# Performance work log

Hardware: AMD Instinct MI355X
Metric: run time of the kernel (lower is better)

Reference implementation:

```python
import jax, jax.numpy as jnp
import numpy as np


def setup_inputs() -> dict:
    key = jax.random.key(0)
    k1, k2, k3 = jax.random.split(key, 3)
    d = 256
    x = jax.random.normal(k1, (8, 2048, d), dtype=jnp.float32)
    # torch nn.Linear(d, d, bias=False) weights, shape [out, in]
    Wq = jax.random.normal(k2, (d, d), dtype=jnp.float32) * (d ** -0.5)
    Wk = jax.random.normal(k3, (d, d), dtype=jnp.float32) * (d ** -0.5)
    return {"x": x, "Wq": Wq, "Wk": Wk}


def reference(x, Wq, Wk):
    # q = x @ Wq^T, k = x @ Wk^T (torch Linear convention), v = x (raw context)
    d = x.shape[-1]
    scale = d ** -0.5
    q = jnp.einsum('bnd,ed->bne', x, Wq)
    k = jnp.einsum('bnd,ed->bne', x, Wk)
    sim = jnp.einsum('bid,bjd->bij', q, k) * scale  # [b, n, n]
    attn = jax.nn.softmax(sim, axis=-1)
    out = jnp.einsum('bij,bjd->bid', attn, x)
    return out
```

## Files before the change

### kernel.cpp

```cpp
#include <hip/hip_runtime.h>
#include <hip/hip_bf16.h>

#define BB 8
#define NN 2048
#define DD 256

typedef _Float16 half8 __attribute__((ext_vector_type(8)));
typedef _Float16 half4 __attribute__((ext_vector_type(4)));
typedef float f32x4 __attribute__((ext_vector_type(4)));
typedef unsigned int uint4v __attribute__((ext_vector_type(4)));

#define GLDS(gsrc, ldst) __builtin_amdgcn_global_load_lds( \
    (const __attribute__((address_space(1))) void*)(gsrc), \
    (__attribute__((address_space(3))) void*)(ldst), 16, 0, 0)

__device__ __forceinline__ half8 cvt8(const float* __restrict__ p) {
    f32x4 a = *(const f32x4*)p;
    f32x4 b = *(const f32x4*)(p + 4);
    half8 h;
    h[0] = (_Float16)a[0]; h[1] = (_Float16)a[1];
    h[2] = (_Float16)a[2]; h[3] = (_Float16)a[3];
    h[4] = (_Float16)b[0]; h[5] = (_Float16)b[1];
    h[6] = (_Float16)b[2]; h[7] = (_Float16)b[3];
    return h;
}

__global__ void __launch_bounds__(256)
qk_proj(const float* __restrict__ x, const float* __restrict__ Wq,
        const float* __restrict__ Wk, _Float16* __restrict__ qh,
        _Float16* __restrict__ kh, _Float16* __restrict__ xT) {
    __shared__ __align__(16) _Float16 Wql[16][264];
    __shared__ __align__(16) _Float16 Wkl[16][264];
    const int tid = threadIdx.x;
    const int wave = tid >> 6, lane = tid & 63;
    const int g = lane >> 4, l16 = lane & 15;
    const int rowblk = blockIdx.x >> 1, thalf = blockIdx.x & 1;
    const size_t r0 = ((size_t)rowblk * 4 + wave) * 16;

    half8 xa[8];
#pragma unroll
    for (int c = 0; c < 8; ++c)
        xa[c] = cvt8(x + (r0 + l16) * DD + c * 32 + g * 8);

    {
        const int gt = (int)(r0 + l16);
        const int bb = gt >> 11, nn = gt & 2047;
        _Float16* xtb = xT + (size_t)bb * DD * NN + nn;
        if (thalf == 0) {
#pragma unroll
            for (int c = 0; c < 4; ++c)
#pragma unroll
                for (int j = 0; j < 8; ++j)
                    xtb[(size_t)(c * 32 + g * 8 + j) * NN] = xa[c][j];
        } else {
#pragma unroll
            for (int c = 4; c < 8; ++c)
#pragma unroll
                for (int j = 0; j < 8; ++j)
                    xtb[(size_t)(c * 32 + g * 8 + j) * NN] = xa[c][j];
        }
    }

    for (int i = 0; i < 8; ++i) {
        const int t = thalf * 8 + i;
        __syncthreads();
        {
            const int sel = tid >> 7;
            const int tt  = tid & 127;
            const int row = tt >> 3;
            const int col = (tt & 7) * 32;
            const float* src = (sel ? Wk : Wq) + (size_t)(t * 16 + row) * DD + col;
            _Float16* dst = sel ? &Wkl[row][col] : &Wql[row][col];
#pragma unroll
            for (int j = 0; j < 4; ++j)
                *(half8*)(dst + j * 8) = cvt8(src + j * 8);
        }
        __syncthreads();
        f32x4 aq = {0.f, 0.f, 0.f, 0.f}, ak = {0.f, 0.f, 0.f, 0.f};
#pragma unroll
        for (int c = 0; c < 8; ++c) {
            half8 bq = *(const half8*)&Wql[l16][c * 32 + g * 8];
            half8 bk = *(const half8*)&Wkl[l16][c * 32 + g * 8];
            aq = __builtin_amdgcn_mfma_f32_16x16x32_f16(xa[c], bq, aq, 0, 0, 0);
            ak = __builtin_amdgcn_mfma_f32_16x16x32_f16(xa[c], bk, ak, 0, 0, 0);
        }
#pragma unroll
        for (int r = 0; r < 4; ++r) {
            size_t row = r0 + g * 4 + r;
            qh[row * DD + t * 16 + l16] = (_Float16)(aq[r] * 0.0625f);
            kh[row * DD + t * 16 + l16] = (_Float16)ak[r];
        }
    }
}

__global__ void __launch_bounds__(512, 2)
attn(const _Float16* __restrict__ qh, const _Float16* __restrict__ kh,
     const _Float16* __restrict__ xT, float* __restrict__ out,
     _Float16* __restrict__ Op, float* __restrict__ ml, int lgS) {
    __shared__ __align__(16) _Float16 Kl[2][32 * 256];
    __shared__ __align__(16) _Float16 Vl[2][256 * 32];
    const int tid = threadIdx.x;
    const int wave = tid >> 6, lane = tid & 63;
    const int g = lane >> 4, l16 = lane & 15;
    const int S = 1 << lgS;
    const int b = blockIdx.x & 7;
    const int tt = blockIdx.x >> 3;
    const int s = tt & (S - 1);
    const int qb = tt >> lgS;
    const int wq0 = qb * 256 + wave * 32;
    const int kvlen = NN >> lgS;
    const int kv_begin = s * kvlen;
    const int nt = kvlen >> 5;

    const _Float16* qp = qh + ((size_t)b * NN + wq0) * DD;
    const _Float16* kb = kh + (size_t)b * NN * DD;
    const _Float16* vb = xT + (size_t)b * DD * NN;

    int krow[2], koff[2], vrow[2];
#pragma unroll
    for (int j = 0; j < 2; ++j) {
        int rp = 8 * j + wave;
        int T = 2 * rp + (lane >> 5);
        krow[j] = 8 * ((T >> 2) & 3) + 4 * (T >> 4) + (T & 3);
        koff[j] = ((lane & 31) * 8) ^ ((T & 7) << 3);
        vrow[j] = 16 * rp + (lane >> 2);
    }
    const int voff = (lane & 3) * 8;

    half8 qf[2][8];
#pragma unroll
    for (int t = 0; t < 2; ++t)
#pragma unroll
        for (int c = 0; c < 8; ++c)
            qf[t][c] = *(const half8*)(qp + (size_t)(t * 16 + l16) * DD + c * 32 + g * 8);

    f32x4 O[2][16];
    f32x4 zero = {0.f, 0.f, 0.f, 0.f};
#pragma unroll
    for (int t = 0; t < 2; ++t)
#pragma unroll
        for (int dt = 0; dt < 16; ++dt) O[t][dt] = zero;
    float m[2] = {-1e30f, -1e30f};
    float l[2] = {0.f, 0.f};
    half8 paA[2], paB[2];

    f32x4 s00, s01, s10, s11;
    auto qkt = [&](int tau) {
        const _Float16* Klb = Kl[tau & 1];
        s00 = zero; s01 = zero; s10 = zero; s11 = zero;
        const int swz = (l16 & 7) << 3;
#pragma unroll
        for (int c = 0; c < 8; ++c) {
            int u = (c * 32 + g * 8) ^ swz;
            half8 k0 = *(const half8*)&Klb[l16 * 256 + u];
            half8 k1 = *(const half8*)&Klb[(16 + l16) * 256 + u];
            s00 = __builtin_amdgcn_mfma_f32_16x16x32_f16(k0, qf[0][c], s00, 0, 0, 0);
            s01 = __builtin_amdgcn_mfma_f32_16x16x32_f16(k1, qf[0][c], s01, 0, 0, 0);
            s10 = __builtin_amdgcn_mfma_f32_16x16x32_f16(k0, qf[1][c], s10, 0, 0, 0);
            s11 = __builtin_amdgcn_mfma_f32_16x16x32_f16(k1, qf[1][c], s11, 0, 0, 0);
        }
    };

    auto pv = [&](int tau, half8 (&paIn)[2]) {
        const _Float16* Vlb = Vl[tau & 1];
#pragma unroll
        for (int dt = 0; dt < 16; ++dt) {
            half8 vf = *(const half8*)&Vlb[(dt * 16 + l16) * 32 + g * 8];
            O[0][dt] = __builtin_amdgcn_mfma_f32_16x16x32_f16(paIn[0], vf, O[0][dt], 0, 0, 0);
            O[1][dt] = __builtin_amdgcn_mfma_f32_16x16x32_f16(paIn[1], vf, O[1][dt], 0, 0, 0);
        }
    };

    auto smax = [&](half8 (&paOut)[2]) {
        float tm[2];
#pragma unroll
        for (int t = 0; t < 2; ++t) {
            const f32x4& a = t ? s10 : s00;
            const f32x4& c = t ? s11 : s01;
            float v = fmaxf(fmaxf(fmaxf(a[0], a[1]), fmaxf(a[2], a[3])),
                            fmaxf(fmaxf(c[0], c[1]), fmaxf(c[2], c[3])));
            v = fmaxf(v, __shfl_xor(v, 16));
            v = fmaxf(v, __shfl_xor(v, 32));
            tm[t] = v;
        }
        bool need = (tm[0] > m[0] + 8.f) || (tm[1] > m[1] + 8.f);
        if (__ballot(need)) {
#pragma unroll
            for (int t = 0; t < 2; ++t) {
                float nm = fmaxf(m[t], tm[t]);
                float al = __expf(m[t] - nm);
                m[t] = nm;
                l[t] *= al;
                float alr[4];
#pragma unroll
                for (int r = 0; r < 4; ++r) alr[r] = __shfl(al, g * 4 + r);
#pragma unroll
                for (int dt = 0; dt < 16; ++dt)
#pragma unroll
                    for (int r = 0; r < 4; ++r) O[t][dt][r] *= alr[r];
            }
        }
#pragma unroll
        for (int t = 0; t < 2; ++t) {
            f32x4 e0, e1;
            const f32x4& a = t ? s10 : s00;
            const f32x4& c = t ? s11 : s01;
#pragma unroll
            for (int r = 0; r < 4; ++r) {
                e0[r] = __expf(a[r] - m[t]);
                e1[r] = __expf(c[r] - m[t]);
            }
            float rs = (e0[0] + e0[1]) + (e0[2] + e0[3]) +
                       (e1[0] + e1[1]) + (e1[2] + e1[3]);
            rs += __shfl_xor(rs, 16);
            rs += __shfl_xor(rs, 32);
            l[t] += rs;

            uint4v w;
            w[0] = __builtin_bit_cast(unsigned, __builtin_amdgcn_cvt_pkrtz(e0[0], e0[1]));
            w[1] = __builtin_bit_cast(unsigned, __builtin_amdgcn_cvt_pkrtz(e0[2], e0[3]));
            w[2] = __builtin_bit_cast(unsigned, __builtin_amdgcn_cvt_pkrtz(e1[0], e1[1]));
            w[3] = __builtin_bit_cast(unsigned, __builtin_amdgcn_cvt_pkrtz(e1[2], e1[3]));
            paOut[t] = __builtin_bit_cast(half8, w);
        }
    };

    auto issueK = [&](int tau) {
        _Float16* kdst = Kl[tau & 1];
        const int kvn = kv_begin + (tau << 5);
#pragma unroll
        for (int j = 0; j < 2; ++j) {
            int rp = 8 * j + wave;
            GLDS(kb + (size_t)(kvn + krow[j]) * DD + koff[j], kdst + rp * 512);
        }
    };
    auto issueV = [&](int tau) {
        _Float16* vdst = Vl[tau & 1];
        const int kvn = kv_begin + (tau << 5);
#pragma unroll
        for (int j = 0; j < 2; ++j) {
            int rp = 8 * j + wave;
            GLDS(vb + (size_t)vrow[j] * NN + kvn + voff, vdst + rp * 512);
        }
    };

    auto body = [&](int tau, half8 (&paIn)[2], half8 (&paOut)[2]) {
        __syncthreads();
        if (tau + 1 < nt) issueK(tau + 1);
        qkt(tau);
        pv(tau - 1, paIn);
        smax(paOut);
        __syncthreads();
        if (tau + 1 < nt) issueV(tau + 1);
    };

    issueK(0); issueV(0);
    __syncthreads();
    issueK(1); issueV(1);
    qkt(0);
    smax(paA);

    int tau = 1;
    for (; tau + 1 < nt - 1; tau += 2) {
        body(tau, paA, paB);
        body(tau + 1, paB, paA);
    }
    body(nt - 1, paA, paB);
    pv(nt - 1, paB);

    if (lgS == 0) {
#pragma unroll
        for (int t = 0; t < 2; ++t) {
            float rl = 1.0f / l[t];
            float rlr[4];
#pragma unroll
            for (int r = 0; r < 4; ++r) rlr[r] = __shfl(rl, g * 4 + r);
            float* ob = out + ((size_t)b * NN + wq0 + t * 16) * DD;
#pragma unroll
            for (int dt = 0; dt < 16; ++dt)
#pragma unroll
                for (int r = 0; r < 4; ++r)
                    ob[(size_t)(g * 4 + r) * DD + dt * 16 + l16] = O[t][dt][r] * rlr[r];
        }
    } else {
#pragma unroll
        for (int t = 0; t < 2; ++t) {
            float rl = 1.0f / l[t];
            float rlr[4];
#pragma unroll
            for (int r = 0; r < 4; ++r) rlr[r] = __shfl(rl, g * 4 + r);
            _Float16* ow = Op + (((size_t)s * BB + b) * NN + wq0 + t * 16) * DD;
#pragma unroll
            for (int dt = 0; dt < 16; ++dt)
#pragma unroll
                for (int r = 0; r < 4; ++r)
                    ow[(dt * 4 + r) * 64 + lane] = (_Float16)(O[t][dt][r] * rlr[r]);
        }
        if (lane < 16) {
            float* mlp = ml + (((size_t)s * BB + b) * NN + wq0) * 2;
#pragma unroll
            for (int t = 0; t < 2; ++t) {
                mlp[(t * 16 + lane) * 2]     = m[t];
                mlp[(t * 16 + lane) * 2 + 1] = l[t];
            }
        }
    }
}

__global__ void __launch_bounds__(256)
combine(const _Float16* __restrict__ Op, const float* __restrict__ ml,
        float* __restrict__ out, int S) {
    const int b = blockIdx.x & 7;
    const int k = blockIdx.x >> 3;
    const int row = b * NN + k * 4 + (threadIdx.x >> 6);
    const int c0  = (threadIdx.x & 63) * 4;
    const int widx = ((c0 >> 4) * 4 + (row & 3)) * 64 + ((row >> 2) & 3) * 16 + (c0 & 15);
    const size_t rbase = (size_t)(row & ~15) * DD + widx;

    float M = -1e30f;
    for (int s = 0; s < S; ++s)
        M = fmaxf(M, ml[((size_t)s * BB * NN + row) * 2]);
    float wsum = 0.f;
    f32x4 acc = {0.f, 0.f, 0.f, 0.f};
    for (int s = 0; s < S; ++s) {
        const float* mlp = ml + ((size_t)s * BB * NN + row) * 2;
        float w = __expf(mlp[0] - M) * mlp[1];
        wsum += w;
        half4 o = *(const half4*)(Op + (size_t)s * BB * NN * DD + rbase);
        acc[0] += w * (float)o[0]; acc[1] += w * (float)o[1];
        acc[2] += w * (float)o[2]; acc[3] += w * (float)o[3];
    }
    float inv = 1.0f / wsum;
    f32x4 res = {acc[0] * inv, acc[1] * inv, acc[2] * inv, acc[3] * inv};
    *(f32x4*)(out + (size_t)row * DD + c0) = res;
}

extern "C" void kernel_launch(void* const* d_in, const int* in_sizes, int n_in,
                              void* d_out, int out_size, void* d_ws, size_t ws_size,
                              hipStream_t stream) {
    const float* x  = (const float*)d_in[0];
    const float* Wq = (const float*)d_in[1];
    const float* Wk = (const float*)d_in[2];
    float* out = (float*)d_out;

    const size_t NTOK = (size_t)BB * NN;
    const size_t HBUF = NTOK * DD * sizeof(_Float16);
    _Float16* qh = (_Float16*)d_ws;
    _Float16* kh = qh + NTOK * DD;
    _Float16* xT = kh + NTOK * DD;
    const size_t base = 3 * HBUF;
    const size_t OSZ  = NTOK * DD * sizeof(_Float16);
    const size_t MLSZ = NTOK * 2 * sizeof(float);

    int lgS = 0;
    if (ws_size >= base + 8 * (OSZ + MLSZ)) lgS = 3;
    else if (ws_size >= base + 4 * (OSZ + MLSZ)) lgS = 2;
    else if (ws_size >= base + 2 * (OSZ + MLSZ)) lgS = 1;
    const int S = 1 << lgS;

    _Float16* Op = (_Float16*)((char*)d_ws + base);
    float* ml = (float*)((char*)d_ws + base + (size_t)S * OSZ);

    qk_proj<<<dim3(BB * NN / 64 * 2), dim3(256), 0, stream>>>(x, Wq, Wk, qh, kh, xT);
    attn<<<dim3(BB * (NN / 256) * S), dim3(512), 0, stream>>>(qh, kh, xT, out, Op, ml, lgS);
    if (S > 1)
        combine<<<dim3(BB * NN / 4), dim3(256), 0, stream>>>(Op, ml, out, S);
}
```

Measured before the change: 107.3 us.

## Halve attention block size, cap KV splits at four, rewrite combine per tile

The attention kernel now runs 4 waves per block covering 128 query rows instead of 8 waves covering 256. Each wave issues twice as many K/V global-to-LDS loads to fill the shared tiles. The KV split count is capped at 4 instead of 8, which reduces partial-output traffic while keeping the grid size similar. The combine kernel is rewritten so each wave handles a 16-row tile: it reads the MFMA-layout partials with contiguous half8 loads and uses shuffles to distribute the per-row weights. The aim is less combine memory traffic and better-coalesced reads, at the cost of more load instructions per wave in attn.

```diff
diff --git a/kernel.cpp b/kernel.cpp
--- a/kernel.cpp
+++ b/kernel.cpp
@@ -93,7 +93,7 @@
     }
 }
 
-__global__ void __launch_bounds__(512, 2)
+__global__ void __launch_bounds__(256, 2)
 attn(const _Float16* __restrict__ qh, const _Float16* __restrict__ kh,
      const _Float16* __restrict__ xT, float* __restrict__ out,
      _Float16* __restrict__ Op, float* __restrict__ ml, int lgS) {
@@ -107,7 +107,7 @@
     const int tt = blockIdx.x >> 3;
     const int s = tt & (S - 1);
     const int qb = tt >> lgS;
-    const int wq0 = qb * 256 + wave * 32;
+    const int wq0 = qb * 128 + wave * 32;
     const int kvlen = NN >> lgS;
     const int kv_begin = s * kvlen;
     const int nt = kvlen >> 5;
@@ -116,10 +116,10 @@
     const _Float16* kb = kh + (size_t)b * NN * DD;
     const _Float16* vb = xT + (size_t)b * DD * NN;
 
-    int krow[2], koff[2], vrow[2];
-#pragma unroll
-    for (int j = 0; j < 2; ++j) {
-        int rp = 8 * j + wave;
+    int krow[4], koff[4], vrow[4];
+#pragma unroll
+    for (int j = 0; j < 4; ++j) {
+        int rp = 4 * j + wave;
         int T = 2 * rp + (lane >> 5);
         krow[j] = 8 * ((T >> 2) & 3) + 4 * (T >> 4) + (T & 3);
         koff[j] = ((lane & 31) * 8) ^ ((T & 7) << 3);
@@ -229,8 +229,8 @@
         _Float16* kdst = Kl[tau & 1];
         const int kvn = kv_begin + (tau << 5);
 #pragma unroll
-        for (int j = 0; j < 2; ++j) {
-            int rp = 8 * j + wave;
+        for (int j = 0; j < 4; ++j) {
+            int rp = 4 * j + wave;
             GLDS(kb + (size_t)(kvn + krow[j]) * DD + koff[j], kdst + rp * 512);
         }
     };
@@ -238,8 +238,8 @@
         _Float16* vdst = Vl[tau & 1];
         const int kvn = kv_begin + (tau << 5);
 #pragma unroll
-        for (int j = 0; j < 2; ++j) {
-            int rp = 8 * j + wave;
+        for (int j = 0; j < 4; ++j) {
+            int rp = 4 * j + wave;
             GLDS(vb + (size_t)vrow[j] * NN + kvn + voff, vdst + rp * 512);
         }
     };
@@ -310,29 +310,50 @@
 __global__ void __launch_bounds__(256)
 combine(const _Float16* __restrict__ Op, const float* __restrict__ ml,
         float* __restrict__ out, int S) {
+    const int tid = threadIdx.x;
+    const int wave = tid >> 6, lane = tid & 63;
     const int b = blockIdx.x & 7;
-    const int k = blockIdx.x >> 3;
-    const int row = b * NN + k * 4 + (threadIdx.x >> 6);
-    const int c0  = (threadIdx.x & 63) * 4;
-    const int widx = ((c0 >> 4) * 4 + (row & 3)) * 64 + ((row >> 2) & 3) * 16 + (c0 & 15);
-    const size_t rbase = (size_t)(row & ~15) * DD + widx;
-
+    const int kk = blockIdx.x >> 3;
+    const int n0 = (kk * 4 + wave) * 16;
+    const size_t NT = (size_t)BB * NN;
+
+    const int q = lane & 15;
+    float ms[4], ls[4];
     float M = -1e30f;
-    for (int s = 0; s < S; ++s)
-        M = fmaxf(M, ml[((size_t)s * BB * NN + row) * 2]);
-    float wsum = 0.f;
-    f32x4 acc = {0.f, 0.f, 0.f, 0.f};
     for (int s = 0; s < S; ++s) {
-        const float* mlp = ml + ((size_t)s * BB * NN + row) * 2;
-        float w = __expf(mlp[0] - M) * mlp[1];
-        wsum += w;
-        half4 o = *(const half4*)(Op + (size_t)s * BB * NN * DD + rbase);
-        acc[0] += w * (float)o[0]; acc[1] += w * (float)o[1];
-        acc[2] += w * (float)o[2]; acc[3] += w * (float)o[3];
-    }
-    float inv = 1.0f / wsum;
-    f32x4 res = {acc[0] * inv, acc[1] * inv, acc[2] * inv, acc[3] * inv};
-    *(f32x4*)(out + (size_t)row * DD + c0) = res;
+        const float* mlp = ml + ((size_t)s * NT + (size_t)b * NN + n0 + q) * 2;
+        ms[s] = mlp[0]; ls[s] = mlp[1];
+        M = fmaxf(M, ms[s]);
+    }
+    float w[4], wsum = 0.f;
+    for (int s = 0; s < S; ++s) { w[s] = __expf(ms[s] - M) * ls[s]; wsum += w[s]; }
+
+    const int qloc = ((lane & 7) >> 1) * 4 + ((lane >> 3) & 3);
+    float wv[4];
+    for (int s = 0; s < S; ++s) wv[s] = __shfl(w[s], qloc);
+    const float inv = 1.0f / __shfl(wsum, qloc);
+
+    const size_t tb = ((size_t)b * NN + n0) * DD;
+    const int dtbase = lane >> 5;
+    const size_t rowg = (size_t)b * NN + n0 + qloc;
+
+    for (int sg = 0; sg < 8; ++sg) {
+        const int off = (sg * 8 + (lane >> 3)) * 64 + (lane & 7) * 8;
+        float acc[8];
+#pragma unroll
+        for (int i = 0; i < 8; ++i) acc[i] = 0.f;
+        for (int s = 0; s < S; ++s) {
+            half8 v = *(const half8*)(Op + (size_t)s * NT * DD + tb + off);
+#pragma unroll
+            for (int i = 0; i < 8; ++i) acc[i] += wv[s] * (float)v[i];
+        }
+        const int dt = sg * 2 + dtbase;
+        float* op = out + rowg * DD + dt * 16 + (lane & 1) * 8;
+        f32x4 r0 = {acc[0] * inv, acc[1] * inv, acc[2] * inv, acc[3] * inv};
+        f32x4 r1 = {acc[4] * inv, acc[5] * inv, acc[6] * inv, acc[7] * inv};
+        *(f32x4*)op = r0;
+        *(f32x4*)(op + 4) = r1;
+    }
 }
 
 extern "C" void kernel_launch(void* const* d_in, const int* in_sizes, int n_in,
@@ -353,8 +374,7 @@
     const size_t MLSZ = NTOK * 2 * sizeof(float);
 
     int lgS = 0;
-    if (ws_size >= base + 8 * (OSZ + MLSZ)) lgS = 3;
-    else if (ws_size >= base + 4 * (OSZ + MLSZ)) lgS = 2;
+    if (ws_size >= base + 4 * (OSZ + MLSZ)) lgS = 2;
     else if (ws_size >= base + 2 * (OSZ + MLSZ)) lgS = 1;
     const int S = 1 << lgS;
 
@@ -362,7 +382,7 @@
     float* ml = (float*)((char*)d_ws + base + (size_t)S * OSZ);
 
     qk_proj<<<dim3(BB * NN / 64 * 2), dim3(256), 0, stream>>>(x, Wq, Wk, qh, kh, xT);
-    attn<<<dim3(BB * (NN / 256) * S), dim3(512), 0, stream>>>(qh, kh, xT, out, Op, ml, lgS);
+    attn<<<dim3(BB * (NN / 128) * S), dim3(256), 0, stream>>>(qh, kh, xT, out, Op, ml, lgS);
     if (S > 1)
-        combine<<<dim3(BB * NN / 4), dim3(256), 0, stream>>>(Op, ml, out, S);
-}
+        combine<<<dim3(BB * NN / 64), dim3(256), 0, stream>>>(Op, ml, out, S);
+}
```

Result: faster. 102.1 us (-4.8%).
